# Optimization experiments

Measured on AMD Instinct MI355X. Metric: run time of the kernel, lower is better.

## Reference

```python
import jax, jax.numpy as jnp
import numpy as np

B, S, D = 2, 1024, 7168
H, HD, RD, QL = 64, 128, 64, 1536
EPS = 1e-6
SOFTMAX_SCALE = HD ** (-0.5)


def _rope_interleave(x, cos, sin):
    """Interleaved RoPE (pairs x[2i], x[2i+1]); x: [T, n, RD], cos/sin: [T, RD]."""
    x1 = x[..., 0::2]
    x2 = x[..., 1::2]
    c = cos[:, None, 0::2]
    s = sin[:, None, 0::2]
    o1 = x1 * c - x2 * s
    o2 = x2 * c + x1 * s
    return jnp.stack([o1, o2], axis=-1).reshape(x.shape)


def setup_inputs() -> dict:
    key = jax.random.key(0)
    ks = jax.random.split(key, 8)
    x = jax.random.normal(ks[0], (B, S, D), dtype=jnp.float32) * 0.02
    qr = jax.random.normal(ks[1], (B * S, QL), dtype=jnp.float32) * 0.02
    # real interleaved-RoPE cos/sin tables, tiled over batch
    pos = jnp.arange(S, dtype=jnp.float32)
    inv_freq = 1.0 / (10000.0 ** (jnp.arange(0, RD, 2, dtype=jnp.float32) / RD))
    freqs = pos[:, None] * inv_freq[None, :]                      # [S, RD/2]
    cos = jnp.repeat(jnp.cos(freqs), 2, axis=-1)                  # [S, RD]
    sin = jnp.repeat(jnp.sin(freqs), 2, axis=-1)
    cos = jnp.tile(cos, (B, 1))                                   # [B*S, RD]
    sin = jnp.tile(sin, (B, 1))
    wq_b_w = jax.random.normal(ks[2], (QL, H * HD), dtype=jnp.float32) * (QL ** -0.5)
    wk_w = jax.random.normal(ks[3], (D, HD), dtype=jnp.float32) * (D ** -0.5)
    wproj_w = jax.random.normal(ks[4], (D, H), dtype=jnp.float32) * (D ** -0.5)
    ln_gamma = jnp.ones((HD,), dtype=jnp.float32)
    ln_beta = jnp.ones((HD,), dtype=jnp.float32)  # module inits bias to ones
    return {"x": x, "qr": qr, "cos": cos, "sin": sin, "wq_b_w": wq_b_w,
            "wk_w": wk_w, "wproj_w": wproj_w, "ln_gamma": ln_gamma, "ln_beta": ln_beta}


def reference(x, qr, cos, sin, wq_b_w, wk_w, wproj_w, ln_gamma, ln_beta):
    b, s, d = x.shape
    t = b * s
    xf = x.reshape(t, d)
    # ---- query path: low-rank up-proj, split rope/nope, interleaved RoPE ----
    q = (qr @ wq_b_w).reshape(t, H, HD)
    q_pe, q_nope = q[..., :RD], q[..., RD:]
    q_pe = _rope_interleave(q_pe, cos, sin)
    q = jnp.concatenate([q_pe, q_nope], axis=-1).reshape(b, s, H, HD)
    # ---- per-head gating weights ----
    w = (xf @ wproj_w).reshape(b, s, H)
    # ---- key path: project, LayerNorm, RoPE on rope slice ----
    kp = xf @ wk_w                                                # [T, HD]
    mu = jnp.mean(kp, axis=-1, keepdims=True)
    var = jnp.mean(jnp.square(kp - mu), axis=-1, keepdims=True)
    kn = (kp - mu) * jax.lax.rsqrt(var + EPS) * ln_gamma + ln_beta
    k_pe, k_nope = kn[..., :RD], kn[..., RD:]
    k_pe = _rope_interleave(k_pe[:, None, :], cos, sin)[:, 0]
    k = jnp.concatenate([k_pe, k_nope], axis=-1).reshape(b, s, HD)
    # ---- lightning-indexer scores: weighted ReLU(q.k) summed over heads ----
    logits = jnp.einsum("bqhd,bkd->bqhk", q, k)                   # [B,S,H,S]
    scores = SOFTMAX_SCALE * jnp.einsum("bqh,bqhk->bqk", w, jax.nn.relu(logits))
    return scores
```

## Files before the change

kernel.cpp:

```cpp
#include <hip/hip_runtime.h>

typedef unsigned short u16;
typedef unsigned int   u32;

typedef __bf16 bf16x8 __attribute__((ext_vector_type(8)));
typedef float  f32x4  __attribute__((ext_vector_type(4)));

__device__ __forceinline__ float bf2f(u16 u){ u32 x = ((u32)u) << 16; return __builtin_bit_cast(float, x); }
__device__ __forceinline__ u16 f2bf(float f){
  u32 u = __builtin_bit_cast(u32, f);
  u32 r = (u + 0x7FFFu + ((u >> 16) & 1u)) >> 16;
  return (u16)r;
}
__device__ __forceinline__ u32 pk2bf(float a, float b){
  u32 ua = __builtin_bit_cast(u32, a) + 0x8000u;
  u32 ub = __builtin_bit_cast(u32, b) + 0x8000u;
  return __builtin_amdgcn_perm(ub, ua, 0x07060302u);
}
__device__ __forceinline__ void glds16(const void* g, void* l){
  __builtin_amdgcn_global_load_lds((const __attribute__((address_space(1))) void*)g,
                                   (__attribute__((address_space(3))) void*)l, 16, 0, 0);
}

__global__ __launch_bounds__(256) void transpose_f32_bf16(const float* __restrict__ src,
                                                          u16* __restrict__ dst, int R, int C){
  __shared__ u16 tile[32][33];
  int c0 = blockIdx.x * 32, r0 = blockIdx.y * 32;
  int tx = threadIdx.x & 31, ty = threadIdx.x >> 5;
  #pragma unroll
  for (int i = ty; i < 32; i += 8) tile[i][tx] = f2bf(src[(size_t)(r0 + i) * C + (c0 + tx)]);
  __syncthreads();
  #pragma unroll
  for (int i = ty; i < 32; i += 8) dst[(size_t)(c0 + i) * R + (r0 + tx)] = tile[tx][i];
}

__global__ __launch_bounds__(256) void cvt_f32_bf16(const float* __restrict__ src,
                                                    u16* __restrict__ dst){
  size_t i = ((size_t)blockIdx.x * 256 + threadIdx.x) * 8;
  const float4* a4 = (const float4*)(src + i);
  float4 f0 = a4[0], f1 = a4[1];
  u32 w[4] = { pk2bf(f0.x, f0.y), pk2bf(f0.z, f0.w), pk2bf(f1.x, f1.y), pk2bf(f1.z, f1.w) };
  *(uint4*)(dst + i) = *(const uint4*)w;
}

__global__ __launch_bounds__(256) void proj_splitk(const float* __restrict__ X,
    const u16* __restrict__ BT, float* __restrict__ P){
  constexpr int Kf = 7168;
  const int s = blockIdx.x, m0 = blockIdx.y * 64;
  const int kbase = s * 448;
  __shared__ u16 As[2 * 64 * 36];
  __shared__ u16 Bs[2 * 192 * 32];
  const int tid = threadIdx.x, wave = tid >> 6, lane = tid & 63;
  const int row = lane & 15, quad = lane >> 4;
  const int wm = (wave & 1) * 32, wn = (wave >> 1) * 96;

  const f32x4 zero = {0.f, 0.f, 0.f, 0.f};
  f32x4 acc[2][6];
  #pragma unroll
  for (int mt = 0; mt < 2; ++mt)
    #pragma unroll
    for (int nt = 0; nt < 6; ++nt) acc[mt][nt] = zero;

  for (int kb = 0; kb < 7; ++kb) {
    int k0 = kbase + kb * 64;
    #pragma unroll
    for (int c = 0; c < 6; ++c) {
      int chunk = wave * 6 + c;
      int kc = chunk / 12, rem = chunk % 12;
      int r = rem * 16 + (lane >> 2), col = (lane & 3) * 8;
      glds16(BT + (size_t)r * Kf + k0 + kc * 32 + col, (void*)&Bs[chunk * 512]);
    }
    #pragma unroll
    for (int c = 0; c < 2; ++c) {
      int idx = tid + c * 256;
      int r = idx >> 3, kf = (idx & 7) * 8;
      const float4* ap = (const float4*)(X + (size_t)(m0 + r) * Kf + k0 + kf);
      float4 f0 = ap[0], f1 = ap[1];
      u32 w[4] = { pk2bf(f0.x, f0.y), pk2bf(f0.z, f0.w), pk2bf(f1.x, f1.y), pk2bf(f1.z, f1.w) };
      *(uint4*)&As[(kf >> 5) * 2304 + r * 36 + (kf & 31)] = *(const uint4*)w;
    }
    __syncthreads();
    #pragma unroll
    for (int ks = 0; ks < 2; ++ks) {
      bf16x8 af[2], bfr[6];
      #pragma unroll
      for (int mt = 0; mt < 2; ++mt) af[mt] = *(const bf16x8*)&As[ks * 2304 + (wm + mt * 16 + row) * 36 + quad * 8];
      #pragma unroll
      for (int nt = 0; nt < 6; ++nt) bfr[nt] = *(const bf16x8*)&Bs[ks * 6144 + (wn + nt * 16 + row) * 32 + quad * 8];
      #pragma unroll
      for (int mt = 0; mt < 2; ++mt)
        #pragma unroll
        for (int nt = 0; nt < 6; ++nt)
          acc[mt][nt] = __builtin_amdgcn_mfma_f32_16x16x32_bf16(af[mt], bfr[nt], acc[mt][nt], 0, 0, 0);
    }
    __syncthreads();
  }
  #pragma unroll
  for (int mt = 0; mt < 2; ++mt)
    #pragma unroll
    for (int nt = 0; nt < 6; ++nt)
      #pragma unroll
      for (int r = 0; r < 4; ++r) {
        int rr = m0 + wm + mt * 16 + quad * 4 + r;
        int cc = wn + nt * 16 + row;
        P[((size_t)s * 2048 + rr) * 192 + cc] = acc[mt][nt][r];
      }
}

__global__ __launch_bounds__(64) void reduce_lnrope(const float* __restrict__ P,
    const float* __restrict__ cosb, const float* __restrict__ sinb,
    const float* __restrict__ gam, const float* __restrict__ bet,
    u16* __restrict__ Kout, float* __restrict__ Wout){
  int tok = blockIdx.x, lane = threadIdx.x;
  float v0 = 0.f, v1 = 0.f, w = 0.f;
  #pragma unroll
  for (int s = 0; s < 16; ++s) {
    const float* p = P + ((size_t)s * 2048 + tok) * 192;
    v0 += p[2 * lane]; v1 += p[2 * lane + 1]; w += p[128 + lane];
  }
  Wout[tok * 64 + lane] = w;
  float sm = v0 + v1;
  #pragma unroll
  for (int m = 1; m < 64; m <<= 1) sm += __shfl_xor(sm, m);
  float mu = sm * (1.f / 128.f);
  float d0 = v0 - mu, d1 = v1 - mu;
  float sq = d0 * d0 + d1 * d1;
  #pragma unroll
  for (int m = 1; m < 64; m <<= 1) sq += __shfl_xor(sq, m);
  float rs = rsqrtf(sq * (1.f / 128.f) + 1e-6f);
  float kn0 = d0 * rs * gam[2 * lane]     + bet[2 * lane];
  float kn1 = d1 * rs * gam[2 * lane + 1] + bet[2 * lane + 1];
  float o0 = kn0, o1 = kn1;
  if (lane < 32) {
    float c  = cosb[tok * 64 + 2 * lane];
    float sn = sinb[tok * 64 + 2 * lane];
    o0 = kn0 * c - kn1 * sn;
    o1 = kn1 * c + kn0 * sn;
  }
  Kout[tok * 128 + 2 * lane]     = f2bf(o0);
  Kout[tok * 128 + 2 * lane + 1] = f2bf(o1);
}

template<bool AGLDS>
__global__ __launch_bounds__(256) void qgemm(const void* __restrict__ Aptr,
    const u16* __restrict__ BT, const float* __restrict__ cosb,
    const float* __restrict__ sinb, u16* __restrict__ Qout){
  constexpr int K = 1536, N = 8192;
  constexpr int LDA = AGLDS ? 32 : 40;
  __shared__ u16 As[128 * LDA];
  __shared__ u16 Bs[128 * 32];
  const int tid = threadIdx.x, wave = tid >> 6, lane = tid & 63;
  const int row = lane & 15, quad = lane >> 4;
  const int wm = (wave >> 1) * 64, wn = (wave & 1) * 64;
  const int m0 = blockIdx.y * 128, n0 = blockIdx.x * 128;

  const f32x4 zero = {0.f, 0.f, 0.f, 0.f};
  f32x4 acc[4][4];
  #pragma unroll
  for (int mt = 0; mt < 4; ++mt)
    #pragma unroll
    for (int nt = 0; nt < 4; ++nt) acc[mt][nt] = zero;

  for (int k0 = 0; k0 < K; k0 += 32) {
    #pragma unroll
    for (int c = 0; c < 2; ++c) {
      int chunk = wave * 2 + c;
      int r = chunk * 16 + (lane >> 2), col = (lane & 3) * 8;
      glds16(BT + (size_t)(n0 + r) * K + k0 + col, (void*)&Bs[chunk * 512]);
    }
    if (AGLDS) {
      #pragma unroll
      for (int c = 0; c < 2; ++c) {
        int chunk = wave * 2 + c;
        int r = chunk * 16 + (lane >> 2), col = (lane & 3) * 8;
        glds16((const u16*)Aptr + (size_t)(m0 + r) * K + k0 + col, (void*)&As[chunk * 512]);
      }
    } else {
      #pragma unroll
      for (int c = 0; c < 2; ++c) {
        int idx = tid + c * 256;
        int r = idx >> 2, kk = (idx & 3) * 8;
        const float4* ap = (const float4*)((const float*)Aptr + (size_t)(m0 + r) * K + k0 + kk);
        float4 f0 = ap[0], f1 = ap[1];
        u32 w[4] = { pk2bf(f0.x, f0.y), pk2bf(f0.z, f0.w), pk2bf(f1.x, f1.y), pk2bf(f1.z, f1.w) };
        *(uint4*)&As[r * LDA + kk] = *(const uint4*)w;
      }
    }
    __syncthreads();
    bf16x8 af[4], bfr[4];
    #pragma unroll
    for (int mt = 0; mt < 4; ++mt) af[mt]  = *(const bf16x8*)&As[(wm + mt * 16 + row) * LDA + quad * 8];
    #pragma unroll
    for (int nt = 0; nt < 4; ++nt) bfr[nt] = *(const bf16x8*)&Bs[(wn + nt * 16 + row) * 32 + quad * 8];
    #pragma unroll
    for (int mt = 0; mt < 4; ++mt)
      #pragma unroll
      for (int nt = 0; nt < 4; ++nt)
        acc[mt][nt] = __builtin_amdgcn_mfma_f32_16x16x32_bf16(af[mt], bfr[nt], acc[mt][nt], 0, 0, 0);
    __syncthreads();
  }

  const bool roped = (wn == 0);
  #pragma unroll
  for (int mt = 0; mt < 4; ++mt)
    #pragma unroll
    for (int nt = 0; nt < 4; ++nt)
      #pragma unroll
      for (int r = 0; r < 4; ++r) {
        int rr = m0 + wm + mt * 16 + quad * 4 + r;
        int cc = n0 + wn + nt * 16 + row;
        float v = acc[mt][nt][r];
        float o = v;
        if (roped) {
          int hd = (wn + nt * 16 + row) & 127;
          float c = cosb[rr * 64 + hd];
          float s = sinb[rr * 64 + hd];
          float vo = __shfl_xor(v, 1);
          o = (cc & 1) ? (v * c + vo * s) : (v * c - vo * s);
        }
        Qout[(size_t)rr * N + cc] = f2bf(o);
      }
}

__global__ __launch_bounds__(256) void attn_kernel(const u16* __restrict__ Q,
    const u16* __restrict__ Kb, const float* __restrict__ Wf, float* __restrict__ out){
  int blk = blockIdx.x;
  int x = blk & 7, kt = (blk >> 3) & 7, hs = (blk >> 6) & 1, g = (blk >> 7) & 3;
  int p = x + 8 * g;
  int b = p >> 4, qt = p & 15;
  int q0 = qt * 64, k0 = kt * 128;

  const int tid = threadIdx.x, wave = tid >> 6, lane = tid & 63;
  const int row = lane & 15, quad = lane >> 4;
  const int wm = (wave >> 1) * 32;
  const int wn = (wave & 1) * 64;

  __shared__ u16 Ks[128 * 136];
  __shared__ u16 Qs[4 * 64 * 32];

  #pragma unroll
  for (int c = 0; c < 8; ++c) {
    int idx = tid + c * 256;
    int rr = idx >> 4, kk = (idx & 15) * 8;
    *(uint4*)&Ks[rr * 136 + kk] = *(const uint4*)(Kb + (size_t)(b * 1024 + k0 + rr) * 128 + kk);
  }
  __syncthreads();

  bf16x8 bfr[4][4];
  #pragma unroll
  for (int ks = 0; ks < 4; ++ks)
    #pragma unroll
    for (int nt = 0; nt < 4; ++nt)
      bfr[ks][nt] = *(const bf16x8*)&Ks[(wn + nt * 16 + row) * 136 + ks * 32 + quad * 8];

  const f32x4 zero = {0.f, 0.f, 0.f, 0.f};
  f32x4 sacc[2][4];
  #pragma unroll
  for (int mt = 0; mt < 2; ++mt)
    #pragma unroll
    for (int nt = 0; nt < 4; ++nt) sacc[mt][nt] = zero;

  for (int hi = 0; hi < 32; ++hi) {
    int h = hs * 32 + hi;
    __syncthreads();
    #pragma unroll
    for (int c = 0; c < 4; ++c) {
      int chunk = wave * 4 + c;
      int kc = chunk >> 2, rg = chunk & 3;
      glds16(Q + (size_t)(b * 1024 + q0 + rg * 16 + (lane >> 2)) * 8192 + h * 128 + kc * 32 + (lane & 3) * 8,
             (void*)&Qs[chunk * 512]);
    }
    __syncthreads();

    f32x4 lg[2][4];
    #pragma unroll
    for (int mt = 0; mt < 2; ++mt)
      #pragma unroll
      for (int nt = 0; nt < 4; ++nt) lg[mt][nt] = zero;
    #pragma unroll
    for (int ks = 0; ks < 4; ++ks) {
      bf16x8 af0 = *(const bf16x8*)&Qs[ks * 2048 + (wm +      row) * 32 + quad * 8];
      bf16x8 af1 = *(const bf16x8*)&Qs[ks * 2048 + (wm + 16 + row) * 32 + quad * 8];
      #pragma unroll
      for (int nt = 0; nt < 4; ++nt) {
        lg[0][nt] = __builtin_amdgcn_mfma_f32_16x16x32_bf16(af0, bfr[ks][nt], lg[0][nt], 0, 0, 0);
        lg[1][nt] = __builtin_amdgcn_mfma_f32_16x16x32_bf16(af1, bfr[ks][nt], lg[1][nt], 0, 0, 0);
      }
    }
    float wv[2][4];
    #pragma unroll
    for (int mt = 0; mt < 2; ++mt)
      #pragma unroll
      for (int r = 0; r < 4; ++r)
        wv[mt][r] = Wf[(size_t)(b * 1024 + q0 + wm + mt * 16 + quad * 4 + r) * 64 + h];
    #pragma unroll
    for (int mt = 0; mt < 2; ++mt)
      #pragma unroll
      for (int nt = 0; nt < 4; ++nt)
        #pragma unroll
        for (int r = 0; r < 4; ++r)
          sacc[mt][nt][r] += wv[mt][r] * fmaxf(lg[mt][nt][r], 0.f);
  }

  const float scale = 0.088388347648318447f;
  #pragma unroll
  for (int mt = 0; mt < 2; ++mt)
    #pragma unroll
    for (int nt = 0; nt < 4; ++nt)
      #pragma unroll
      for (int r = 0; r < 4; ++r) {
        int qq = q0 + wm + mt * 16 + quad * 4 + r;
        int kk = k0 + wn + nt * 16 + row;
        unsafeAtomicAdd(&out[((size_t)b << 20) + (size_t)qq * 1024 + kk], scale * sacc[mt][nt][r]);
      }
}

extern "C" void kernel_launch(void* const* d_in, const int* in_sizes, int n_in,
                              void* d_out, int out_size, void* d_ws, size_t ws_size,
                              hipStream_t stream) {
  const float* x    = (const float*)d_in[0];
  const float* qr   = (const float*)d_in[1];
  const float* cosb = (const float*)d_in[2];
  const float* sinb = (const float*)d_in[3];
  const float* wq   = (const float*)d_in[4];
  const float* wk   = (const float*)d_in[5];
  const float* wp   = (const float*)d_in[6];
  const float* gam  = (const float*)d_in[7];
  const float* bet  = (const float*)d_in[8];
  float* out = (float*)d_out;

  char* ws = (char*)d_ws;
  float* P    = (float*)(ws + 0);
  u16*   wqT  = (u16*)(ws + 0);
  u16*   wkwpT= (u16*)(ws + 25165824);
  float* Wf   = (float*)(ws + 27918336);
  u16*   Kbf  = (u16*)(ws + 28442624);
  u16*   Qbf  = (u16*)(ws + 28966912);
  const size_t QRB_OFF = 62521344;
  u16*   qrb  = (u16*)(ws + QRB_OFF);
  const bool big_ws = (ws_size >= (size_t)68812800);

  (void)in_sizes; (void)n_in;

  hipMemsetAsync(d_out, 0, (size_t)out_size * 4, stream);

  transpose_f32_bf16<<<dim3(4, 224),  256, 0, stream>>>(wk, wkwpT,              7168, 128);
  transpose_f32_bf16<<<dim3(2, 224),  256, 0, stream>>>(wp, wkwpT + 128 * 7168, 7168, 64);

  proj_splitk<<<dim3(16, 32), 256, 0, stream>>>(x, wkwpT, P);
  reduce_lnrope<<<2048, 64, 0, stream>>>(P, cosb, sinb, gam, bet, Kbf, Wf);

  transpose_f32_bf16<<<dim3(256, 48), 256, 0, stream>>>(wq, wqT, 1536, 8192);

  if (big_ws) {
    cvt_f32_bf16<<<1536, 256, 0, stream>>>(qr, qrb);
    qgemm<true><<<dim3(64, 16), 256, 0, stream>>>(qrb, wqT, cosb, sinb, Qbf);
  } else {
    qgemm<false><<<dim3(64, 16), 256, 0, stream>>>(qr, wqT, cosb, sinb, Qbf);
  }

  attn_kernel<<<512, 256, 0, stream>>>(Qbf, Kbf, Wf, out);
}
```

Baseline: 342.5 us.

## Deepen qgemm K-step, batch two heads per attn iteration, stage transposed weights in LDS

The Q GEMM now loads a 64-wide K slab per barrier pair (two 32-wide sub-slabs) instead of 32, which halves the number of sync rounds. The scoring kernel loads K through global_load_lds into a shared buffer that it reuses for Q, processes two heads per sync round, and stages the per-head gate weights in LDS from a head-major transposed layout written by the reduce kernel. These changes aim to cut barrier overhead and scattered global weight loads. The trade-off is more LDS use, and the padded K layout that avoided bank conflicts is dropped.

```diff
diff --git a/kernel.cpp b/kernel.cpp
--- a/kernel.cpp
+++ b/kernel.cpp
@@ -110,7 +110,7 @@
 __global__ __launch_bounds__(64) void reduce_lnrope(const float* __restrict__ P,
     const float* __restrict__ cosb, const float* __restrict__ sinb,
     const float* __restrict__ gam, const float* __restrict__ bet,
-    u16* __restrict__ Kout, float* __restrict__ Wout){
+    u16* __restrict__ Kout, float* __restrict__ WoutT){
   int tok = blockIdx.x, lane = threadIdx.x;
   float v0 = 0.f, v1 = 0.f, w = 0.f;
   #pragma unroll
@@ -118,7 +118,7 @@
     const float* p = P + ((size_t)s * 2048 + tok) * 192;
     v0 += p[2 * lane]; v1 += p[2 * lane + 1]; w += p[128 + lane];
   }
-  Wout[tok * 64 + lane] = w;
+  WoutT[(size_t)lane * 2048 + tok] = w;
   float sm = v0 + v1;
   #pragma unroll
   for (int m = 1; m < 64; m <<= 1) sm += __shfl_xor(sm, m);
@@ -146,9 +146,8 @@
     const u16* __restrict__ BT, const float* __restrict__ cosb,
     const float* __restrict__ sinb, u16* __restrict__ Qout){
   constexpr int K = 1536, N = 8192;
-  constexpr int LDA = AGLDS ? 32 : 40;
-  __shared__ u16 As[128 * LDA];
-  __shared__ u16 Bs[128 * 32];
+  __shared__ u16 As[2 * 128 * 32];
+  __shared__ u16 Bs[2 * 128 * 32];
   const int tid = threadIdx.x, wave = tid >> 6, lane = tid & 63;
   const int row = lane & 15, quad = lane >> 4;
   const int wm = (wave >> 1) * 64, wn = (wave & 1) * 64;
@@ -161,42 +160,47 @@
     #pragma unroll
     for (int nt = 0; nt < 4; ++nt) acc[mt][nt] = zero;
 
-  for (int k0 = 0; k0 < K; k0 += 32) {
-    #pragma unroll
-    for (int c = 0; c < 2; ++c) {
-      int chunk = wave * 2 + c;
-      int r = chunk * 16 + (lane >> 2), col = (lane & 3) * 8;
+  for (int k0 = 0; k0 < K; k0 += 64) {
+    #pragma unroll
+    for (int c = 0; c < 4; ++c) {
+      int chunk = wave * 4 + c;
+      int kc = chunk >> 3, rg = chunk & 7;
+      int r = rg * 16 + (lane >> 2), col = kc * 32 + (lane & 3) * 8;
       glds16(BT + (size_t)(n0 + r) * K + k0 + col, (void*)&Bs[chunk * 512]);
     }
     if (AGLDS) {
       #pragma unroll
-      for (int c = 0; c < 2; ++c) {
-        int chunk = wave * 2 + c;
-        int r = chunk * 16 + (lane >> 2), col = (lane & 3) * 8;
+      for (int c = 0; c < 4; ++c) {
+        int chunk = wave * 4 + c;
+        int kc = chunk >> 3, rg = chunk & 7;
+        int r = rg * 16 + (lane >> 2), col = kc * 32 + (lane & 3) * 8;
         glds16((const u16*)Aptr + (size_t)(m0 + r) * K + k0 + col, (void*)&As[chunk * 512]);
       }
     } else {
       #pragma unroll
-      for (int c = 0; c < 2; ++c) {
+      for (int c = 0; c < 4; ++c) {
         int idx = tid + c * 256;
-        int r = idx >> 2, kk = (idx & 3) * 8;
-        const float4* ap = (const float4*)((const float*)Aptr + (size_t)(m0 + r) * K + k0 + kk);
+        int r = idx >> 3, kf = (idx & 7) * 8;
+        const float4* ap = (const float4*)((const float*)Aptr + (size_t)(m0 + r) * K + k0 + kf);
         float4 f0 = ap[0], f1 = ap[1];
         u32 w[4] = { pk2bf(f0.x, f0.y), pk2bf(f0.z, f0.w), pk2bf(f1.x, f1.y), pk2bf(f1.z, f1.w) };
-        *(uint4*)&As[r * LDA + kk] = *(const uint4*)w;
-      }
-    }
-    __syncthreads();
-    bf16x8 af[4], bfr[4];
-    #pragma unroll
-    for (int mt = 0; mt < 4; ++mt) af[mt]  = *(const bf16x8*)&As[(wm + mt * 16 + row) * LDA + quad * 8];
-    #pragma unroll
-    for (int nt = 0; nt < 4; ++nt) bfr[nt] = *(const bf16x8*)&Bs[(wn + nt * 16 + row) * 32 + quad * 8];
-    #pragma unroll
-    for (int mt = 0; mt < 4; ++mt)
-      #pragma unroll
-      for (int nt = 0; nt < 4; ++nt)
-        acc[mt][nt] = __builtin_amdgcn_mfma_f32_16x16x32_bf16(af[mt], bfr[nt], acc[mt][nt], 0, 0, 0);
+        *(uint4*)&As[(kf >> 5) * 4096 + r * 32 + (kf & 31)] = *(const uint4*)w;
+      }
+    }
+    __syncthreads();
+    #pragma unroll
+    for (int kk = 0; kk < 2; ++kk) {
+      bf16x8 af[4], bfr[4];
+      #pragma unroll
+      for (int mt = 0; mt < 4; ++mt) af[mt]  = *(const bf16x8*)&As[kk * 4096 + (wm + mt * 16 + row) * 32 + quad * 8];
+      #pragma unroll
+      for (int nt = 0; nt < 4; ++nt) bfr[nt] = *(const bf16x8*)&Bs[kk * 4096 + (wn + nt * 16 + row) * 32 + quad * 8];
+      #pragma unroll
+      for (int mt = 0; mt < 4; ++mt)
+        #pragma unroll
+        for (int nt = 0; nt < 4; ++nt)
+          acc[mt][nt] = __builtin_amdgcn_mfma_f32_16x16x32_bf16(af[mt], bfr[nt], acc[mt][nt], 0, 0, 0);
+    }
     __syncthreads();
   }
 
@@ -223,10 +227,10 @@
 }
 
 __global__ __launch_bounds__(256) void attn_kernel(const u16* __restrict__ Q,
-    const u16* __restrict__ Kb, const float* __restrict__ Wf, float* __restrict__ out){
+    const u16* __restrict__ Kb, const float* __restrict__ WT, float* __restrict__ out){
   int blk = blockIdx.x;
-  int x = blk & 7, kt = (blk >> 3) & 7, hs = (blk >> 6) & 1, g = (blk >> 7) & 3;
-  int p = x + 8 * g;
+  int x = blk & 7, kt = (blk >> 3) & 7, hs = (blk >> 6) & 1, g4 = (blk >> 7) & 3;
+  int p = x + 8 * g4;
   int b = p >> 4, qt = p & 15;
   int q0 = qt * 64, k0 = kt * 128;
 
@@ -235,14 +239,20 @@
   const int wm = (wave >> 1) * 32;
   const int wn = (wave & 1) * 64;
 
-  __shared__ u16 Ks[128 * 136];
-  __shared__ u16 Qs[4 * 64 * 32];
+  __shared__ u16 Sh[2 * 64 * 128];
+  __shared__ float Ws[32 * 64];
 
   #pragma unroll
   for (int c = 0; c < 8; ++c) {
-    int idx = tid + c * 256;
-    int rr = idx >> 4, kk = (idx & 15) * 8;
-    *(uint4*)&Ks[rr * 136 + kk] = *(const uint4*)(Kb + (size_t)(b * 1024 + k0 + rr) * 128 + kk);
+    int g = wave * 8 + c;
+    int rr = g * 4 + (lane >> 4), col = (lane & 15) * 8;
+    glds16(Kb + (size_t)(b * 1024 + k0 + rr) * 128 + col, (void*)&Sh[g * 512]);
+  }
+  {
+    int hl = tid >> 3, qq = (tid & 7) * 8;
+    const float* src = WT + (size_t)(hs * 32 + hl) * 2048 + b * 1024 + q0 + qq;
+    *(float4*)&Ws[hl * 64 + qq]     = *(const float4*)src;
+    *(float4*)&Ws[hl * 64 + qq + 4] = *(const float4*)(src + 4);
   }
   __syncthreads();
 
@@ -251,7 +261,7 @@
   for (int ks = 0; ks < 4; ++ks)
     #pragma unroll
     for (int nt = 0; nt < 4; ++nt)
-      bfr[ks][nt] = *(const bf16x8*)&Ks[(wn + nt * 16 + row) * 136 + ks * 32 + quad * 8];
+      bfr[ks][nt] = *(const bf16x8*)&Sh[(wn + nt * 16 + row) * 128 + ks * 32 + quad * 8];
 
   const f32x4 zero = {0.f, 0.f, 0.f, 0.f};
   f32x4 sacc[2][4];
@@ -260,46 +270,47 @@
     #pragma unroll
     for (int nt = 0; nt < 4; ++nt) sacc[mt][nt] = zero;
 
-  for (int hi = 0; hi < 32; ++hi) {
-    int h = hs * 32 + hi;
-    __syncthreads();
-    #pragma unroll
-    for (int c = 0; c < 4; ++c) {
-      int chunk = wave * 4 + c;
-      int kc = chunk >> 2, rg = chunk & 3;
-      glds16(Q + (size_t)(b * 1024 + q0 + rg * 16 + (lane >> 2)) * 8192 + h * 128 + kc * 32 + (lane & 3) * 8,
-             (void*)&Qs[chunk * 512]);
-    }
-    __syncthreads();
-
-    f32x4 lg[2][4];
-    #pragma unroll
-    for (int mt = 0; mt < 2; ++mt)
-      #pragma unroll
-      for (int nt = 0; nt < 4; ++nt) lg[mt][nt] = zero;
-    #pragma unroll
-    for (int ks = 0; ks < 4; ++ks) {
-      bf16x8 af0 = *(const bf16x8*)&Qs[ks * 2048 + (wm +      row) * 32 + quad * 8];
-      bf16x8 af1 = *(const bf16x8*)&Qs[ks * 2048 + (wm + 16 + row) * 32 + quad * 8];
-      #pragma unroll
-      for (int nt = 0; nt < 4; ++nt) {
-        lg[0][nt] = __builtin_amdgcn_mfma_f32_16x16x32_bf16(af0, bfr[ks][nt], lg[0][nt], 0, 0, 0);
-        lg[1][nt] = __builtin_amdgcn_mfma_f32_16x16x32_bf16(af1, bfr[ks][nt], lg[1][nt], 0, 0, 0);
-      }
-    }
-    float wv[2][4];
-    #pragma unroll
-    for (int mt = 0; mt < 2; ++mt)
-      #pragma unroll
-      for (int r = 0; r < 4; ++r)
-        wv[mt][r] = Wf[(size_t)(b * 1024 + q0 + wm + mt * 16 + quad * 4 + r) * 64 + h];
-    #pragma unroll
-    for (int mt = 0; mt < 2; ++mt)
+  for (int hp = 0; hp < 16; ++hp) {
+    int h0 = hs * 32 + hp * 2;
+    __syncthreads();
+    #pragma unroll
+    for (int c = 0; c < 8; ++c) {
+      int g = wave * 8 + c;
+      int hsub = g >> 4, rem = g & 15;
+      int kc = rem >> 2, rg = rem & 3;
+      glds16(Q + (size_t)(b * 1024 + q0 + rg * 16 + (lane >> 2)) * 8192 + (h0 + hsub) * 128 + kc * 32 + (lane & 3) * 8,
+             (void*)&Sh[hsub * 8192 + rem * 512]);
+    }
+    __syncthreads();
+
+    #pragma unroll
+    for (int hsub = 0; hsub < 2; ++hsub) {
+      f32x4 lg[2][4];
+      #pragma unroll
+      for (int mt = 0; mt < 2; ++mt)
+        #pragma unroll
+        for (int nt = 0; nt < 4; ++nt) lg[mt][nt] = zero;
+      #pragma unroll
+      for (int ks = 0; ks < 4; ++ks) {
+        bf16x8 af0 = *(const bf16x8*)&Sh[hsub * 8192 + ks * 2048 + (wm +      row) * 32 + quad * 8];
+        bf16x8 af1 = *(const bf16x8*)&Sh[hsub * 8192 + ks * 2048 + (wm + 16 + row) * 32 + quad * 8];
+        #pragma unroll
+        for (int nt = 0; nt < 4; ++nt) {
+          lg[0][nt] = __builtin_amdgcn_mfma_f32_16x16x32_bf16(af0, bfr[ks][nt], lg[0][nt], 0, 0, 0);
+          lg[1][nt] = __builtin_amdgcn_mfma_f32_16x16x32_bf16(af1, bfr[ks][nt], lg[1][nt], 0, 0, 0);
+        }
+      }
+      int hl = hp * 2 + hsub;
+      f32x4 w0 = *(const f32x4*)&Ws[hl * 64 + wm +      quad * 4];
+      f32x4 w1 = *(const f32x4*)&Ws[hl * 64 + wm + 16 + quad * 4];
       #pragma unroll
       for (int nt = 0; nt < 4; ++nt)
         #pragma unroll
-        for (int r = 0; r < 4; ++r)
-          sacc[mt][nt][r] += wv[mt][r] * fmaxf(lg[mt][nt][r], 0.f);
+        for (int r = 0; r < 4; ++r) {
+          sacc[0][nt][r] += w0[r] * fmaxf(lg[0][nt][r], 0.f);
+          sacc[1][nt][r] += w1[r] * fmaxf(lg[1][nt][r], 0.f);
+        }
+    }
   }
 
   const float scale = 0.088388347648318447f;
@@ -333,7 +344,7 @@
   float* P    = (float*)(ws + 0);
   u16*   wqT  = (u16*)(ws + 0);
   u16*   wkwpT= (u16*)(ws + 25165824);
-  float* Wf   = (float*)(ws + 27918336);
+  float* WT   = (float*)(ws + 27918336);
   u16*   Kbf  = (u16*)(ws + 28442624);
   u16*   Qbf  = (u16*)(ws + 28966912);
   const size_t QRB_OFF = 62521344;
@@ -348,7 +359,7 @@
   transpose_f32_bf16<<<dim3(2, 224),  256, 0, stream>>>(wp, wkwpT + 128 * 7168, 7168, 64);
 
   proj_splitk<<<dim3(16, 32), 256, 0, stream>>>(x, wkwpT, P);
-  reduce_lnrope<<<2048, 64, 0, stream>>>(P, cosb, sinb, gam, bet, Kbf, Wf);
+  reduce_lnrope<<<2048, 64, 0, stream>>>(P, cosb, sinb, gam, bet, Kbf, WT);
 
   transpose_f32_bf16<<<dim3(256, 48), 256, 0, stream>>>(wq, wqT, 1536, 8192);
 
@@ -359,5 +370,5 @@
     qgemm<false><<<dim3(64, 16), 256, 0, stream>>>(qr, wqT, cosb, sinb, Qbf);
   }
 
-  attn_kernel<<<512, 256, 0, stream>>>(Qbf, Kbf, Wf, out);
-}
+  attn_kernel<<<512, 256, 0, stream>>>(Qbf, Kbf, WT, out);
+}
```

After: 333.8 us. -2.5%, faster.
